# Kernel tuning notes

Hardware: AMD Instinct MI355X
Metric: run time of the kernel (lower is better)

The kernel has to match this reference:

```python
import jax, jax.numpy as jnp
import numpy as np
import math

B, T, C, H = 4, 4096, 512, 64  # batch, seq_len, n_embed, head_size


def setup_inputs() -> dict:
    key = jax.random.key(0)
    kx, kq, kk, kv = jax.random.split(key, 4)
    scale = 1.0 / math.sqrt(C)  # ~Linear init scale
    return {
        "x": jax.random.normal(kx, (B, T, C), dtype=jnp.float32),
        "Wq": jax.random.normal(kq, (C, H), dtype=jnp.float32) * scale,
        "Wk": jax.random.normal(kk, (C, H), dtype=jnp.float32) * scale,
        "Wv": jax.random.normal(kv, (C, H), dtype=jnp.float32) * scale,
    }


def reference(x, Wq, Wk, Wv):
    # Single-head causal self-attention (mask=True path, dropout=0/eval).
    # NOTE: original module scales by 1/sqrt(C) (n_embed), not 1/sqrt(head_size).
    Bn, Tn, Cn = x.shape
    q = x @ Wq  # [B,T,H]
    k = x @ Wk  # [B,T,H]
    v = x @ Wv  # [B,T,H]
    inv_scale = jnp.float32(1.0 / math.sqrt(Cn))
    scores = jnp.einsum('bth,bsh->bts', q, k) * inv_scale  # [B,T,T]
    causal = jnp.tril(jnp.ones((Tn, Tn), dtype=bool))
    scores = jnp.where(causal, scores, jnp.float32(-jnp.inf))
    attn = jax.nn.softmax(scores, axis=-1)
    out = jnp.einsum('bts,bsh->bth', attn, v)  # [B,T,H]
    return out
```

## Files before the change

kernel.cpp:

```cpp
#include <hip/hip_runtime.h>
#include <math.h>

#define BATCH 4
#define SEQT  4096
#define CDIM  512
#define HDIM  64

typedef unsigned short ushort_t;
typedef __attribute__((ext_vector_type(8))) short bf16x8;
typedef __attribute__((ext_vector_type(4))) float f32x4;

#define MFMA16(a, b, c) __builtin_amdgcn_mfma_f32_16x16x32_bf16((a), (b), (c), 0, 0, 0)
#define NEG (-1e30f)

__device__ __forceinline__ ushort_t f2bf(float f) {
  union { float f; unsigned int u; } v;
  v.f = f;
  unsigned int u = v.u;
  u += 0x7fffu + ((u >> 16) & 1u);
  return (ushort_t)(u >> 16);
}
__device__ __forceinline__ unsigned int pk2(float a, float b) {
  return (unsigned int)f2bf(a) | ((unsigned int)f2bf(b) << 16);
}

__global__ __launch_bounds__(256) void convert_w(
    const float* __restrict__ Wq, const float* __restrict__ Wk,
    const float* __restrict__ Wv, ushort_t* __restrict__ wtf) {
  int g = blockIdx.x * 256 + threadIdx.x;
  int lane = g & 63;
  int nt = (g >> 6) & 3;
  int ks = (g >> 8) & 15;
  int mat = g >> 12;
  const float* W = (mat == 0) ? Wq : (mat == 1) ? Wk : Wv;
  const float sc = (mat == 0) ? 0.04419417382415922f : 1.0f;
  int n = lane & 15, quad = lane >> 4;
  int h = nt * 16 + n;
  int c0 = ks * 32 + quad * 8;
  ushort_t tmp[8];
#pragma unroll
  for (int j = 0; j < 8; ++j) tmp[j] = f2bf(W[(c0 + j) * HDIM + h] * sc);
  *(bf16x8*)(wtf + (size_t)g * 8) = *(const bf16x8*)tmp;
}

#define XP 520

__global__ __launch_bounds__(384) void qkv_proj(
    const float* __restrict__ x, const ushort_t* __restrict__ wtf,
    ushort_t* __restrict__ qbf, ushort_t* __restrict__ kbf,
    ushort_t* __restrict__ vbf) {
  __shared__ ushort_t Xs[16 * XP];
  __shared__ float Facc[3 * 1088];
  __shared__ ushort_t Pk[3][16 * 72];

  const int tid = threadIdx.x;
  const int row0 = blockIdx.x * 16;

  const float4* xg = (const float4*)(x + (size_t)row0 * CDIM);
  for (int i = tid; i < 16 * (CDIM / 4); i += 384) {
    float4 xv = xg[i];
    int r = i >> 7, c4 = i & 127;
    uint2 u;
    u.x = pk2(xv.x, xv.y);
    u.y = pk2(xv.z, xv.w);
    *(uint2*)&Xs[r * XP + c4 * 4] = u;
  }
  __syncthreads();

  const int lane = tid & 63;
  const int w = tid >> 6;
  const int mat = w >> 1;
  const int kh = w & 1;
  const int n = lane & 15, quad = lane >> 4;
  const ushort_t* wb = wtf + mat * 32768;

  f32x4 acc[4];
#pragma unroll
  for (int nt = 0; nt < 4; ++nt) acc[nt] = (f32x4){0.f, 0.f, 0.f, 0.f};

  bf16x8 bcur[4];
#pragma unroll
  for (int nt = 0; nt < 4; ++nt)
    bcur[nt] = *(const bf16x8*)&wb[(kh * 8 * 4 + nt) * 512 + lane * 8];

  for (int kk = 0; kk < 8; ++kk) {
    const int ks = kh * 8 + kk;
    bf16x8 a = *(const bf16x8*)&Xs[n * XP + ks * 32 + quad * 8];
    bf16x8 bnext[4];
    if (kk < 7) {
#pragma unroll
      for (int nt = 0; nt < 4; ++nt)
        bnext[nt] = *(const bf16x8*)&wb[((ks + 1) * 4 + nt) * 512 + lane * 8];
    }
#pragma unroll
    for (int nt = 0; nt < 4; ++nt) acc[nt] = MFMA16(a, bcur[nt], acc[nt]);
    if (kk < 7) {
#pragma unroll
      for (int nt = 0; nt < 4; ++nt) bcur[nt] = bnext[nt];
    }
  }

  if (kh == 1) {
#pragma unroll
    for (int nt = 0; nt < 4; ++nt)
#pragma unroll
      for (int i = 0; i < 4; ++i)
        Facc[mat * 1088 + lane * 17 + nt * 4 + i] = acc[nt][i];
  }
  __syncthreads();

  if (kh == 0) {
#pragma unroll
    for (int nt = 0; nt < 4; ++nt)
#pragma unroll
      for (int i = 0; i < 4; ++i) {
        acc[nt][i] += Facc[mat * 1088 + lane * 17 + nt * 4 + i];
        Pk[mat][(quad * 4 + i) * 72 + nt * 16 + n] = f2bf(acc[nt][i]);
      }
    if (mat == 0) {
#pragma unroll
      for (int ks2 = 0; ks2 < 2; ++ks2) {
        bf16x8 fr = *(const bf16x8*)&Pk[0][n * 72 + ks2 * 32 + quad * 8];
        *(bf16x8*)(qbf + (size_t)((row0 >> 4) * 2 + ks2) * 512 + lane * 8) = fr;
      }
    } else if (mat == 1) {
#pragma unroll
      for (int ks2 = 0; ks2 < 2; ++ks2) {
        bf16x8 fr = *(const bf16x8*)&Pk[1][n * 72 + ks2 * 32 + quad * 8];
        *(bf16x8*)(kbf + (size_t)((row0 >> 4) * 2 + ks2) * 512 + lane * 8) = fr;
      }
    } else {
      const int b = row0 >> 12, t0 = row0 & 4095;
      const int kt = t0 >> 6, kslot = (t0 >> 5) & 1, tsub = (t0 >> 4) & 1;
      if ((quad >> 1) == tsub) {
        const int lq = quad & 1;
#pragma unroll
        for (int nt = 0; nt < 4; ++nt) {
          ushort_t tmp[8];
#pragma unroll
          for (int j = 0; j < 8; ++j)
            tmp[j] = Pk[2][(lq * 8 + j) * 72 + nt * 16 + n];
          *(bf16x8*)(vbf + (size_t)(((b * 64 + kt) * 4 + nt) * 2 + kslot) * 512 +
                     lane * 8) = *(const bf16x8*)tmp;
        }
      }
    }
  }
}

__global__ __launch_bounds__(512, 4) void attn(
    const ushort_t* __restrict__ qbf, const ushort_t* __restrict__ kbf,
    const ushort_t* __restrict__ vbf, float* __restrict__ out) {
  __shared__ __align__(16) char smem[35328];
  ushort_t* Ps = (ushort_t*)smem;
  float* Om = (float*)smem;
  float* Ol = (float*)(smem + 34816);

  const int tid = threadIdx.x;
  const int lane = tid & 63;
  const int w = tid >> 6;
  const int m2 = w & 1;
  const int kt0 = w >> 1;
  const int n = lane & 15, quad = lane >> 4;

  const int b = blockIdx.x & 3;
  const int qt = 127 - (blockIdx.x >> 2);
  const int q0 = qt * 32;

  const ushort_t* qB = qbf + (size_t)b * 512 * 512;
  const ushort_t* kB = kbf + (size_t)b * 512 * 512;
  const ushort_t* vB = vbf + (size_t)b * 512 * 512;
  float* oB = out + (size_t)b * SEQT * HDIM;

  bf16x8 qf[2];
#pragma unroll
  for (int ks = 0; ks < 2; ++ks)
    qf[ks] = *(const bf16x8*)&qB[(size_t)((qt * 2 + m2) * 2 + ks) * 512 +
                                 lane * 8];

  bf16x8 ones;
#pragma unroll
  for (int j = 0; j < 8; ++j) ones[j] = (short)0x3F80;

  f32x4 o[4], ol;
#pragma unroll
  for (int nt = 0; nt < 4; ++nt) o[nt] = (f32x4){0.f, 0.f, 0.f, 0.f};
  ol = (f32x4){0.f, 0.f, 0.f, 0.f};

  const int ktiles = (q0 + 95) >> 6;
  ushort_t* Pw = Ps + w * 1152;

  bf16x8 kf[8];
  if (kt0 < ktiles) {
#pragma unroll
    for (int ks = 0; ks < 2; ++ks)
#pragma unroll
      for (int nt = 0; nt < 4; ++nt)
        kf[ks * 4 + nt] = *(const bf16x8*)&kB[(size_t)((kt0 * 4 + nt) * 2 + ks) *
                                                  512 + lane * 8];
  }

  for (int kt = kt0; kt < ktiles; kt += 4) {
    const int k0 = kt * 64;
    const int ktn = kt + 4;

    bf16x8 kfn[8];
    if (ktn < ktiles) {
#pragma unroll
      for (int ks = 0; ks < 2; ++ks)
#pragma unroll
        for (int nt = 0; nt < 4; ++nt)
          kfn[ks * 4 + nt] =
              *(const bf16x8*)&kB[(size_t)((ktn * 4 + nt) * 2 + ks) * 512 +
                                  lane * 8];
    }

    f32x4 s[4];
#pragma unroll
    for (int nt = 0; nt < 4; ++nt) s[nt] = (f32x4){0.f, 0.f, 0.f, 0.f};
#pragma unroll
    for (int ks = 0; ks < 2; ++ks)
#pragma unroll
      for (int nt = 0; nt < 4; ++nt)
        s[nt] = MFMA16(qf[ks], kf[ks * 4 + nt], s[nt]);

    bf16x8 vf[8];
#pragma unroll
    for (int ks = 0; ks < 2; ++ks)
#pragma unroll
      for (int nt = 0; nt < 4; ++nt)
        vf[ks * 4 + nt] = *(const bf16x8*)&vB[(size_t)((kt * 4 + nt) * 2 + ks) *
                                                  512 + lane * 8];

    if (k0 + 63 > q0) {
      const int rbase = q0 + m2 * 16 + quad * 4;
#pragma unroll
      for (int nt = 0; nt < 4; ++nt) {
        const int col = k0 + nt * 16 + n;
#pragma unroll
        for (int i = 0; i < 4; ++i)
          if (col > rbase + i) s[nt][i] = NEG;
      }
    }

#pragma unroll
    for (int nt = 0; nt < 4; ++nt)
#pragma unroll
      for (int i = 0; i < 4; ++i)
        Pw[(quad * 4 + i) * 72 + nt * 16 + n] = f2bf(__expf(s[nt][i]));

#pragma unroll
    for (int ks = 0; ks < 2; ++ks) {
      bf16x8 pa = *(const bf16x8*)&Pw[n * 72 + ks * 32 + quad * 8];
      ol = MFMA16(pa, ones, ol);
#pragma unroll
      for (int nt = 0; nt < 4; ++nt)
        o[nt] = MFMA16(pa, vf[ks * 4 + nt], o[nt]);
    }

#pragma unroll
    for (int f = 0; f < 8; ++f) kf[f] = kfn[f];
  }

  __syncthreads();

  float* OmW = Om + w * 1088;
#pragma unroll
  for (int nt = 0; nt < 4; ++nt)
#pragma unroll
    for (int i = 0; i < 4; ++i)
      OmW[(quad * 4 + i) * 68 + nt * 16 + n] = o[nt][i];
  if (n == 0)
#pragma unroll
    for (int i = 0; i < 4; ++i) Ol[w * 16 + quad * 4 + i] = ol[i];
  __syncthreads();

  {
    const int r = tid >> 4;
    const int c0 = (tid & 15) * 4;
    const int m2r = r >> 4, lr = r & 15;
    float ax = 0.f, ay = 0.f, az = 0.f, aw = 0.f, ls = 0.f;
#pragma unroll
    for (int ww = 0; ww < 4; ++ww) {
      const int wi = m2r + ww * 2;
      const float4 vv = *(const float4*)&Om[wi * 1088 + lr * 68 + c0];
      ax += vv.x; ay += vv.y; az += vv.z; aw += vv.w;
      ls += Ol[wi * 16 + lr];
    }
    const float inv = 1.0f / ls;
    *(float4*)&oB[(size_t)(q0 + r) * HDIM + c0] =
        make_float4(ax * inv, ay * inv, az * inv, aw * inv);
  }
}

extern "C" void kernel_launch(void* const* d_in, const int* in_sizes, int n_in,
                              void* d_out, int out_size, void* d_ws, size_t ws_size,
                              hipStream_t stream) {
  const float* x = (const float*)d_in[0];
  const float* Wq = (const float*)d_in[1];
  const float* Wk = (const float*)d_in[2];
  const float* Wv = (const float*)d_in[3];
  float* out = (float*)d_out;

  ushort_t* wtf = (ushort_t*)d_ws;
  ushort_t* qbf = wtf + 3 * 16 * 4 * 512;
  ushort_t* kbf = qbf + (size_t)BATCH * 512 * 512;
  ushort_t* vbf = kbf + (size_t)BATCH * 512 * 512;

  convert_w<<<48, 256, 0, stream>>>(Wq, Wk, Wv, wtf);
  qkv_proj<<<BATCH * SEQT / 16, 384, 0, stream>>>(x, wtf, qbf, kbf, vbf);
  attn<<<512, 512, 0, stream>>>(qbf, kbf, vbf, out);
}
```

Measured before the change: 117.1 us.

## XOR-swizzle LDS tiles and reorder K/V loads to cut register pressure

Replaces the padded LDS layouts (row pitch 520/72) with unpadded 512/64 rows using an XOR swizzle on 16-byte chunks, for both the x tile in the projection and the P tile in attention. The aim is to avoid bank conflicts without padding. The attention loop now overwrites the K fragments in place after the QK MFMAs instead of double-buffering them in a separate array. V loads are split into two halves issued around the prefetch. This lowers live VGPRs and may improve occupancy, at the risk of less latency hiding for the K prefetch.

Result: slower. 161.2 us (+37.7%).

```diff
diff --git a/kernel.cpp b/kernel.cpp
--- a/kernel.cpp
+++ b/kernel.cpp
@@ -43,15 +43,13 @@
   *(bf16x8*)(wtf + (size_t)g * 8) = *(const bf16x8*)tmp;
 }
 
-#define XP 520
-
 __global__ __launch_bounds__(384) void qkv_proj(
     const float* __restrict__ x, const ushort_t* __restrict__ wtf,
     ushort_t* __restrict__ qbf, ushort_t* __restrict__ kbf,
     ushort_t* __restrict__ vbf) {
-  __shared__ ushort_t Xs[16 * XP];
+  __shared__ ushort_t Xs[16 * 512];
   __shared__ float Facc[3 * 1088];
-  __shared__ ushort_t Pk[3][16 * 72];
+  __shared__ ushort_t Pk[3][16 * 64];
 
   const int tid = threadIdx.x;
   const int row0 = blockIdx.x * 16;
@@ -60,10 +58,11 @@
   for (int i = tid; i < 16 * (CDIM / 4); i += 384) {
     float4 xv = xg[i];
     int r = i >> 7, c4 = i & 127;
+    int chunk = (c4 >> 1) ^ (r & 7);
     uint2 u;
     u.x = pk2(xv.x, xv.y);
     u.y = pk2(xv.z, xv.w);
-    *(uint2*)&Xs[r * XP + c4 * 4] = u;
+    *(uint2*)&Xs[r * 512 + chunk * 8 + (c4 & 1) * 4] = u;
   }
   __syncthreads();
 
@@ -85,7 +84,7 @@
 
   for (int kk = 0; kk < 8; ++kk) {
     const int ks = kh * 8 + kk;
-    bf16x8 a = *(const bf16x8*)&Xs[n * XP + ks * 32 + quad * 8];
+    bf16x8 a = *(const bf16x8*)&Xs[n * 512 + ((4 * ks + quad) ^ (n & 7)) * 8];
     bf16x8 bnext[4];
     if (kk < 7) {
 #pragma unroll
@@ -115,19 +114,17 @@
 #pragma unroll
       for (int i = 0; i < 4; ++i) {
         acc[nt][i] += Facc[mat * 1088 + lane * 17 + nt * 4 + i];
-        Pk[mat][(quad * 4 + i) * 72 + nt * 16 + n] = f2bf(acc[nt][i]);
-      }
-    if (mat == 0) {
+        const int row = quad * 4 + i;
+        Pk[mat][row * 64 + (((2 * nt + (n >> 3)) ^ (row & 7)) * 8) + (n & 7)] =
+            f2bf(acc[nt][i]);
+      }
+    if (mat < 2) {
+      ushort_t* dst = (mat == 0) ? qbf : kbf;
 #pragma unroll
       for (int ks2 = 0; ks2 < 2; ++ks2) {
-        bf16x8 fr = *(const bf16x8*)&Pk[0][n * 72 + ks2 * 32 + quad * 8];
-        *(bf16x8*)(qbf + (size_t)((row0 >> 4) * 2 + ks2) * 512 + lane * 8) = fr;
-      }
-    } else if (mat == 1) {
-#pragma unroll
-      for (int ks2 = 0; ks2 < 2; ++ks2) {
-        bf16x8 fr = *(const bf16x8*)&Pk[1][n * 72 + ks2 * 32 + quad * 8];
-        *(bf16x8*)(kbf + (size_t)((row0 >> 4) * 2 + ks2) * 512 + lane * 8) = fr;
+        bf16x8 fr = *(const bf16x8*)&Pk[mat][n * 64 +
+                                            (((4 * ks2 + quad) ^ (n & 7)) * 8)];
+        *(bf16x8*)(dst + (size_t)((row0 >> 4) * 2 + ks2) * 512 + lane * 8) = fr;
       }
     } else {
       const int b = row0 >> 12, t0 = row0 & 4095;
@@ -138,8 +135,11 @@
         for (int nt = 0; nt < 4; ++nt) {
           ushort_t tmp[8];
 #pragma unroll
-          for (int j = 0; j < 8; ++j)
-            tmp[j] = Pk[2][(lq * 8 + j) * 72 + nt * 16 + n];
+          for (int j = 0; j < 8; ++j) {
+            const int row = lq * 8 + j;
+            tmp[j] = Pk[2][row * 64 +
+                           (((2 * nt + (n >> 3)) ^ (row & 7)) * 8) + (n & 7)];
+          }
           *(bf16x8*)(vbf + (size_t)(((b * 64 + kt) * 4 + nt) * 2 + kslot) * 512 +
                      lane * 8) = *(const bf16x8*)tmp;
         }
@@ -188,7 +188,7 @@
   ol = (f32x4){0.f, 0.f, 0.f, 0.f};
 
   const int ktiles = (q0 + 95) >> 6;
-  ushort_t* Pw = Ps + w * 1152;
+  ushort_t* Pw = Ps + w * 1024;
 
   bf16x8 kf[8];
   if (kt0 < ktiles) {
@@ -202,35 +202,38 @@
 
   for (int kt = kt0; kt < ktiles; kt += 4) {
     const int k0 = kt * 64;
+
+    bf16x8 vfa[4];
+#pragma unroll
+    for (int nt = 0; nt < 4; ++nt)
+      vfa[nt] = *(const bf16x8*)&vB[(size_t)((kt * 4 + nt) * 2 + 0) * 512 +
+                                    lane * 8];
+
+    f32x4 s[4];
+#pragma unroll
+    for (int nt = 0; nt < 4; ++nt) s[nt] = (f32x4){0.f, 0.f, 0.f, 0.f};
+#pragma unroll
+    for (int ks = 0; ks < 2; ++ks)
+#pragma unroll
+      for (int nt = 0; nt < 4; ++nt)
+        s[nt] = MFMA16(qf[ks], kf[ks * 4 + nt], s[nt]);
+
     const int ktn = kt + 4;
-
-    bf16x8 kfn[8];
     if (ktn < ktiles) {
 #pragma unroll
       for (int ks = 0; ks < 2; ++ks)
 #pragma unroll
         for (int nt = 0; nt < 4; ++nt)
-          kfn[ks * 4 + nt] =
+          kf[ks * 4 + nt] =
               *(const bf16x8*)&kB[(size_t)((ktn * 4 + nt) * 2 + ks) * 512 +
                                   lane * 8];
     }
 
-    f32x4 s[4];
-#pragma unroll
-    for (int nt = 0; nt < 4; ++nt) s[nt] = (f32x4){0.f, 0.f, 0.f, 0.f};
-#pragma unroll
-    for (int ks = 0; ks < 2; ++ks)
-#pragma unroll
-      for (int nt = 0; nt < 4; ++nt)
-        s[nt] = MFMA16(qf[ks], kf[ks * 4 + nt], s[nt]);
-
-    bf16x8 vf[8];
-#pragma unroll
-    for (int ks = 0; ks < 2; ++ks)
-#pragma unroll
-      for (int nt = 0; nt < 4; ++nt)
-        vf[ks * 4 + nt] = *(const bf16x8*)&vB[(size_t)((kt * 4 + nt) * 2 + ks) *
-                                                  512 + lane * 8];
+    bf16x8 vfb[4];
+#pragma unroll
+    for (int nt = 0; nt < 4; ++nt)
+      vfb[nt] = *(const bf16x8*)&vB[(size_t)((kt * 4 + nt) * 2 + 1) * 512 +
+                                    lane * 8];
 
     if (k0 + 63 > q0) {
       const int rbase = q0 + m2 * 16 + quad * 4;
@@ -246,20 +249,20 @@
 #pragma unroll
     for (int nt = 0; nt < 4; ++nt)
 #pragma unroll
-      for (int i = 0; i < 4; ++i)
-        Pw[(quad * 4 + i) * 72 + nt * 16 + n] = f2bf(__expf(s[nt][i]));
-
-#pragma unroll
-    for (int ks = 0; ks < 2; ++ks) {
-      bf16x8 pa = *(const bf16x8*)&Pw[n * 72 + ks * 32 + quad * 8];
-      ol = MFMA16(pa, ones, ol);
-#pragma unroll
-      for (int nt = 0; nt < 4; ++nt)
-        o[nt] = MFMA16(pa, vf[ks * 4 + nt], o[nt]);
-    }
-
-#pragma unroll
-    for (int f = 0; f < 8; ++f) kf[f] = kfn[f];
+      for (int i = 0; i < 4; ++i) {
+        const int row = quad * 4 + i;
+        Pw[row * 64 + (((2 * nt + (n >> 3)) ^ (row & 7)) * 8) + (n & 7)] =
+            f2bf(__expf(s[nt][i]));
+      }
+
+    bf16x8 pa0 = *(const bf16x8*)&Pw[n * 64 + ((quad ^ (n & 7)) * 8)];
+    bf16x8 pa1 = *(const bf16x8*)&Pw[n * 64 + (((4 + quad) ^ (n & 7)) * 8)];
+    ol = MFMA16(pa0, ones, ol);
+    ol = MFMA16(pa1, ones, ol);
+#pragma unroll
+    for (int nt = 0; nt < 4; ++nt) o[nt] = MFMA16(pa0, vfa[nt], o[nt]);
+#pragma unroll
+    for (int nt = 0; nt < 4; ++nt) o[nt] = MFMA16(pa1, vfb[nt], o[nt]);
   }
 
   __syncthreads();
```
